# Performance work log

Hardware: AMD Instinct MI355X
Metric: run time of the kernel (lower is better)

Reference implementation:

```python
import jax, jax.numpy as jnp
import numpy as np

N = 100000   # nodes
E = 1200000  # edges
NIN, EIN = 6, 1
HID, L, H = 64, 3, 4
D = HID // H  # 16 per-head dim


def setup_inputs() -> dict:
    key = jax.random.key(0)
    ks = jax.random.split(key, 20)
    r = lambda k, shape: (jax.random.normal(k, shape, dtype=jnp.float32) * 0.1)
    inp = {
        "x": jax.random.normal(ks[0], (N, NIN), dtype=jnp.float32),
        "edge_index": jax.random.randint(ks[1], (2, E), 0, N, dtype=jnp.int64),
        "edge_attr": jax.random.normal(ks[2], (E, EIN), dtype=jnp.float32),
        # node encoder (Linear-ReLU-Linear)
        "w_ne1": r(ks[3], (NIN, HID)), "b_ne1": jnp.zeros((HID,), jnp.float32),
        "w_ne2": r(ks[4], (HID, HID)), "b_ne2": jnp.zeros((HID,), jnp.float32),
        # edge encoder (Linear)
        "w_ee": r(ks[5], (EIN, HID)), "b_ee": jnp.zeros((HID,), jnp.float32),
        # stacked GAT layers (PyG GATConv w/ edge features, concat heads)
        "w_gat": r(ks[6], (L, HID, HID)),      # node lin per layer
        "w_eg": r(ks[7], (L, HID, HID)),       # edge lin per layer
        "att_src": r(ks[8], (L, H, D)),
        "att_dst": r(ks[9], (L, H, D)),
        "att_edge": r(ks[10], (L, H, D)),
        "b_gat": jnp.zeros((L, HID), jnp.float32),
        # per-layer LayerNorm
        "ln_g": jnp.ones((L, HID), jnp.float32),
        "ln_b": jnp.zeros((L, HID), jnp.float32),
        # output projection
        "w_out": r(ks[11], (HID, HID)), "b_out": jnp.zeros((HID,), jnp.float32),
    }
    return inp


def _layernorm(x, g, b, eps=1e-5):
    m = jnp.mean(x, axis=-1, keepdims=True)
    v = jnp.mean(jnp.square(x - m), axis=-1, keepdims=True)
    return (x - m) * jax.lax.rsqrt(v + eps) * g + b


def reference(x, edge_index, edge_attr, w_ne1, b_ne1, w_ne2, b_ne2, w_ee, b_ee,
              w_gat, w_eg, att_src, att_dst, att_edge, b_gat, ln_g, ln_b,
              w_out, b_out):
    n = x.shape[0]
    src, dst = edge_index[0], edge_index[1]
    # encode nodes / edges
    h = jax.nn.relu(x @ w_ne1 + b_ne1) @ w_ne2 + b_ne2          # [N, HID]
    e = edge_attr @ w_ee + b_ee                                  # [E, HID]
    num_layers = w_gat.shape[0]
    for l in range(num_layers):
        hw = (h @ w_gat[l]).reshape(n, H, D)                     # [N,H,D]
        ew = (e @ w_eg[l]).reshape(-1, H, D)                     # [E,H,D]
        a_s = jnp.sum(hw * att_src[l], axis=-1)                  # [N,H]
        a_d = jnp.sum(hw * att_dst[l], axis=-1)                  # [N,H]
        a_e = jnp.sum(ew * att_edge[l], axis=-1)                 # [E,H]
        score = jax.nn.leaky_relu(a_s[src] + a_d[dst] + a_e, 0.2)  # [E,H]
        # softmax over incoming edges of each destination node
        smax = jax.ops.segment_max(score, dst, num_segments=n)
        ex = jnp.exp(score - smax[dst])
        den = jax.ops.segment_sum(ex, dst, num_segments=n)
        alpha = ex / (den[dst] + 1e-16)                          # [E,H]
        msg = alpha[:, :, None] * hw[src]                        # [E,H,D]
        agg = jax.ops.segment_sum(msg, dst, num_segments=n)      # [N,H,D]
        agg = agg.reshape(n, H * D) + b_gat[l]
        h = _layernorm(h + jax.nn.elu(agg), ln_g[l], ln_b[l])
    return h @ w_out + b_out
```

## Files before the change

### kernel.cpp

```cpp
#include <hip/hip_runtime.h>
#include <hip/hip_bf16.h>

#define NIN 6
#define HIDN 64
#define NHEAD 4
#define DEGPAD 5

__device__ __forceinline__ unsigned short f2bf(float f) {
    unsigned u = __float_as_uint(f);
    unsigned r = (u >> 16) & 1u;
    return (unsigned short)((u + 0x7fffu + r) >> 16);
}

__global__ __launch_bounds__(256) void encode1_kernel(
    const float* __restrict__ x,
    const float* __restrict__ w1, const float* __restrict__ b1,
    float* __restrict__ hid, int N) {
    int t = blockIdx.x * blockDim.x + threadIdx.x;
    int n = t >> 6, j = t & 63;
    if (n >= N) return;
    float acc = b1[j];
#pragma unroll
    for (int i = 0; i < NIN; i++) acc += x[n * NIN + i] * w1[i * HIDN + j];
    hid[(size_t)n * HIDN + j] = acc > 0.f ? acc : 0.f;
}

__global__ __launch_bounds__(256) void mm64_plain_kernel(
    const float* __restrict__ src, const float* __restrict__ W,
    const float* __restrict__ bias, float* __restrict__ dst, int N) {
    int j = threadIdx.x & 63;
    int wv = (blockIdx.x * blockDim.x + threadIdx.x) >> 6;
    int nw = (gridDim.x * blockDim.x) >> 6;

    float Wc[HIDN];
#pragma unroll
    for (int k = 0; k < HIDN; k++) Wc[k] = W[k * HIDN + j];
    float bj = bias[j];

    for (int n0 = wv; n0 < N; n0 += nw) {
        int n = __builtin_amdgcn_readfirstlane(n0);
        const float4* __restrict__ row = (const float4*)(src + (size_t)n * HIDN);
        float a0 = 0.f, a1 = 0.f, a2 = 0.f, a3 = 0.f;
#pragma unroll
        for (int kk = 0; kk < 16; kk++) {
            float4 r = row[kk];
            a0 += r.x * Wc[4 * kk];
            a1 += r.y * Wc[4 * kk + 1];
            a2 += r.z * Wc[4 * kk + 2];
            a3 += r.w * Wc[4 * kk + 3];
        }
        dst[(size_t)n * HIDN + j] = ((a0 + a1) + (a2 + a3)) + bj;
    }
}

__global__ __launch_bounds__(256) void mm64_attn_kernel(
    const float* __restrict__ src, const float* __restrict__ W,
    const float* __restrict__ att_s, const float* __restrict__ att_d,
    unsigned short* __restrict__ dst16,
    float* __restrict__ a_s, float* __restrict__ a_d, int N) {
    int j = threadIdx.x & 63;
    int wv = (blockIdx.x * blockDim.x + threadIdx.x) >> 6;
    int nw = (gridDim.x * blockDim.x) >> 6;

    float Wc[HIDN];
#pragma unroll
    for (int k = 0; k < HIDN; k++) Wc[k] = W[k * HIDN + j];
    float asj = att_s[j];
    float adj = att_d[j];

    for (int n0 = wv; n0 < N; n0 += nw) {
        int n = __builtin_amdgcn_readfirstlane(n0);
        const float4* __restrict__ row = (const float4*)(src + (size_t)n * HIDN);
        float a0 = 0.f, a1 = 0.f, a2 = 0.f, a3 = 0.f;
#pragma unroll
        for (int kk = 0; kk < 16; kk++) {
            float4 r = row[kk];
            a0 += r.x * Wc[4 * kk];
            a1 += r.y * Wc[4 * kk + 1];
            a2 += r.z * Wc[4 * kk + 2];
            a3 += r.w * Wc[4 * kk + 3];
        }
        float acc = (a0 + a1) + (a2 + a3);
        dst16[(size_t)n * HIDN + j] = f2bf(acc);
        float ts = acc * asj;
        float td = acc * adj;
#pragma unroll
        for (int o = 8; o > 0; o >>= 1) {
            ts += __shfl_xor(ts, o);
            td += __shfl_xor(td, o);
        }
        if ((j & 15) == 0) {
            a_s[(size_t)n * NHEAD + (j >> 4)] = ts;
            a_d[(size_t)n * NHEAD + (j >> 4)] = td;
        }
    }
}

__global__ void consts_kernel(const float* __restrict__ w_ee, const float* __restrict__ b_ee,
                              const float* __restrict__ w_eg, const float* __restrict__ att_edge,
                              float* __restrict__ c1, float* __restrict__ c0) {
    int t = threadIdx.x;
    if (t >= 12) return;
    int l = t >> 2, hh = t & 3;
    float s1 = 0.f, s0 = 0.f;
    for (int j = 0; j < HIDN; j++) {
        float wj = 0.f;
        for (int d = 0; d < 16; d++)
            wj += w_eg[l * 4096 + j * 64 + hh * 16 + d] * att_edge[l * 64 + hh * 16 + d];
        s1 += w_ee[j] * wj;
        s0 += b_ee[j] * wj;
    }
    c1[l * 4 + hh] = s1;
    c0[l * 4 + hh] = s0;
}

__global__ __launch_bounds__(256) void hist_kernel(const int* __restrict__ ei,
                                                   unsigned* __restrict__ deg,
                                                   unsigned* __restrict__ rank, int E) {
    int e = blockIdx.x * 256 + threadIdx.x;
    if (e < E) rank[e] = atomicAdd(&deg[(size_t)ei[E + e] << DEGPAD], 1u);
}

__global__ __launch_bounds__(256) void scan1_kernel(const unsigned* __restrict__ deg,
                                                    unsigned* __restrict__ rp,
                                                    unsigned* __restrict__ bsum, int N) {
    __shared__ unsigned sm[256];
    int t = threadIdx.x, i = blockIdx.x * 256 + t;
    unsigned v = (i < N) ? deg[(size_t)i << DEGPAD] : 0u;
    sm[t] = v;
    __syncthreads();
    unsigned x = v;
    for (int o = 1; o < 256; o <<= 1) {
        unsigned add = (t >= o) ? sm[t - o] : 0u;
        __syncthreads();
        x += add; sm[t] = x;
        __syncthreads();
    }
    if (i < N) rp[i] = x - v;
    if (t == 255) bsum[blockIdx.x] = x;
}

__global__ void scan2_kernel(const unsigned* __restrict__ bsum,
                             unsigned* __restrict__ boff, int nb) {
    __shared__ unsigned sm[1024];
    int t = threadIdx.x;
    unsigned v = (t < nb) ? bsum[t] : 0u;
    sm[t] = v;
    __syncthreads();
    unsigned x = v;
    for (int o = 1; o < 1024; o <<= 1) {
        unsigned add = (t >= o) ? sm[t - o] : 0u;
        __syncthreads();
        x += add; sm[t] = x;
        __syncthreads();
    }
    if (t < nb) boff[t] = x - v;
}

__global__ __launch_bounds__(256) void scan3_kernel(unsigned* __restrict__ rp,
                                                    const unsigned* __restrict__ boff,
                                                    int N, int E) {
    int i = blockIdx.x * 256 + threadIdx.x;
    if (i < N) rp[i] = rp[i] + boff[blockIdx.x];
    if (i == 0) rp[N] = (unsigned)E;
}

__global__ __launch_bounds__(256) void csr_scatter_kernel(
    const int* __restrict__ ei, const float* __restrict__ eattr,
    const unsigned* __restrict__ rp, const unsigned* __restrict__ rank,
    int2* __restrict__ eca, int E) {
    int e = blockIdx.x * 256 + threadIdx.x;
    if (e >= E) return;
    int s = ei[e], d = ei[E + e];
    unsigned p = rp[d] + rank[e];
    eca[p] = make_int2(s, __float_as_int(eattr[e]));
}

__global__ __launch_bounds__(256) void gat_fused_kernel(
    const unsigned* __restrict__ rp, const int2* __restrict__ eca,
    const unsigned short* __restrict__ hw16,
    const float* __restrict__ a_s, const float* __restrict__ a_d,
    const float* __restrict__ c1, const float* __restrict__ c0,
    float* __restrict__ h, const float* __restrict__ bg,
    const float* __restrict__ g, const float* __restrict__ b, int N) {
    __shared__ float exl[4 * 272];
    __shared__ int srl[4 * 68];
    int t = blockIdx.x * blockDim.x + threadIdx.x;
    int lane = t & 63;
    int q = lane >> 4;
    int l = lane & 15;
    int hd = l >> 2;
    int sub = l & 3;
    int n = ((t >> 6) << 2) + q;
    int wslot = (threadIdx.x >> 6);
    float* myex = exl + wslot * 272 + 68 * q;
    int* mysrc = srl + wslot * 68 + 17 * q;

    bool nv = n < N;
    unsigned beg = nv ? rp[n] : 0u;
    int deg = nv ? (int)(rp[n + 1] - beg) : 0;

    float4 ad4 = nv ? *(const float4*)(a_d + ((size_t)n << 2)) : make_float4(0, 0, 0, 0);
    float4 C1 = *(const float4*)c1;
    float4 C0 = *(const float4*)c0;

    int md = deg;
    md = max(md, __shfl_xor(md, 16));
    md = max(md, __shfl_xor(md, 32));
    int chunks = (md + 15) >> 4;

    const unsigned* __restrict__ hwp = (const unsigned*)hw16;
    unsigned loff = (unsigned)(l << 1);

    float ssum = 0.f;
    float ac0 = 0.f, ac1 = 0.f, ac2 = 0.f, ac3 = 0.f;

    for (int k = 0; k < chunks; k++) {
        int i = (k << 4) + l;
        bool act = i < deg;
        int2 ce = act ? eca[beg + i] : make_int2(0, 0);
        int src = ce.x;
        float ea = __int_as_float(ce.y);
        float4 as4 = act ? *(const float4*)(a_s + ((size_t)src << 2))
                         : make_float4(0, 0, 0, 0);
        float s0 = as4.x + ad4.x + ea * C1.x + C0.x;
        float s1 = as4.y + ad4.y + ea * C1.y + C0.y;
        float s2 = as4.z + ad4.z + ea * C1.z + C0.z;
        float s3 = as4.w + ad4.w + ea * C1.w + C0.w;
        s0 = s0 >= 0.f ? s0 : 0.2f * s0;
        s1 = s1 >= 0.f ? s1 : 0.2f * s1;
        s2 = s2 >= 0.f ? s2 : 0.2f * s2;
        s3 = s3 >= 0.f ? s3 : 0.2f * s3;
        float e0 = act ? __expf(s0) : 0.f;
        float e1 = act ? __expf(s1) : 0.f;
        float e2 = act ? __expf(s2) : 0.f;
        float e3 = act ? __expf(s3) : 0.f;
        *(float4*)(myex + (l << 2)) = make_float4(e0, e1, e2, e3);
        mysrc[l] = act ? src : 0;

        float w0 = myex[(sub << 2) + hd];
        float w1 = myex[((sub + 4) << 2) + hd];
        float w2 = myex[((sub + 8) << 2) + hd];
        float w3 = myex[((sub + 12) << 2) + hd];
        float csum = (w0 + w1) + (w2 + w3);
        csum += __shfl_xor(csum, 1);
        csum += __shfl_xor(csum, 2);
        ssum += csum;

#pragma unroll
        for (int e = 0; e < 16; e++) {
            float w = myex[(e << 2) + hd];
            int so = mysrc[e];
            uint2 uu = *(const uint2*)(hwp + (((unsigned)so << 5) + loff));
            ac0 += w * __uint_as_float(uu.x << 16);
            ac1 += w * __uint_as_float(uu.x & 0xffff0000u);
            ac2 += w * __uint_as_float(uu.y << 16);
            ac3 += w * __uint_as_float(uu.y & 0xffff0000u);
        }
    }

    if (!nv) return;
    float inv = 1.f / (ssum + 1e-16f);
    float4 bg4 = *(const float4*)(bg + (l << 2));
    float4 hv4 = *(const float4*)(h + (size_t)n * HIDN + (l << 2));

    float a0 = ac0 * inv + bg4.x;
    float a1 = ac1 * inv + bg4.y;
    float a2 = ac2 * inv + bg4.z;
    float a3 = ac3 * inv + bg4.w;
    a0 = a0 > 0.f ? a0 : (__expf(a0) - 1.f);
    a1 = a1 > 0.f ? a1 : (__expf(a1) - 1.f);
    a2 = a2 > 0.f ? a2 : (__expf(a2) - 1.f);
    a3 = a3 > 0.f ? a3 : (__expf(a3) - 1.f);
    float v0 = hv4.x + a0, v1 = hv4.y + a1, v2 = hv4.z + a2, v3 = hv4.w + a3;

    float s = (v0 + v1) + (v2 + v3);
    float sq = (v0 * v0 + v1 * v1) + (v2 * v2 + v3 * v3);
#pragma unroll
    for (int o = 8; o > 0; o >>= 1) {
        s += __shfl_xor(s, o);
        sq += __shfl_xor(sq, o);
    }
    float mean = s * (1.f / 64.f);
    float var = sq * (1.f / 64.f) - mean * mean;
    float rr = rsqrtf(var + 1e-5f);
    float4 g4 = *(const float4*)(g + (l << 2));
    float4 b4 = *(const float4*)(b + (l << 2));
    float4 outv;
    outv.x = (v0 - mean) * rr * g4.x + b4.x;
    outv.y = (v1 - mean) * rr * g4.y + b4.y;
    outv.z = (v2 - mean) * rr * g4.z + b4.z;
    outv.w = (v3 - mean) * rr * g4.w + b4.w;
    *(float4*)(h + (size_t)n * HIDN + (l << 2)) = outv;
}

extern "C" void kernel_launch(void* const* d_in, const int* in_sizes, int n_in,
                              void* d_out, int out_size, void* d_ws, size_t ws_size,
                              hipStream_t stream) {
    const float* x      = (const float*)d_in[0];
    const int*   ei     = (const int*)d_in[1];
    const float* eattr  = (const float*)d_in[2];
    const float* w_ne1  = (const float*)d_in[3];
    const float* b_ne1  = (const float*)d_in[4];
    const float* w_ne2  = (const float*)d_in[5];
    const float* b_ne2  = (const float*)d_in[6];
    const float* w_ee   = (const float*)d_in[7];
    const float* b_ee   = (const float*)d_in[8];
    const float* w_gat  = (const float*)d_in[9];
    const float* w_eg   = (const float*)d_in[10];
    const float* att_src= (const float*)d_in[11];
    const float* att_dst= (const float*)d_in[12];
    const float* att_edge=(const float*)d_in[13];
    const float* b_gat  = (const float*)d_in[14];
    const float* ln_g   = (const float*)d_in[15];
    const float* ln_b   = (const float*)d_in[16];
    const float* w_out  = (const float*)d_in[17];
    const float* b_out  = (const float*)d_in[18];

    const int N = in_sizes[0] / NIN;
    const int E = in_sizes[2];

    float* ws   = (float*)d_ws;
    float* h    = ws;
    float* hid  = h + (size_t)N * 64;
    unsigned short* hw16 = (unsigned short*)(hid + (size_t)N * 64);
    float* a_s  = (float*)(hw16 + (size_t)N * 64);
    float* a_d  = a_s + (size_t)N * 4;
    float* c1   = a_d + (size_t)N * 4;
    float* c0   = c1 + 12;
    int2*  eca  = (int2*)(c0 + 12);
    unsigned* rank = (unsigned*)(eca + (size_t)E);
    unsigned* deg  = rank + (size_t)E;
    unsigned* rp   = deg + ((size_t)N << DEGPAD);
    unsigned* bsum = rp + (size_t)N + 1;
    unsigned* boff = bsum + 1024;

    dim3 blk(256);
    int nodeWaveBlocks = (int)(((size_t)N * 64 + 255) / 256);
    int quadBlocks = (int)(((size_t)((N + 3) / 4) * 64 + 255) / 256);
    int edgeBlocks = (E + 255) / 256;
    int nodeBlocks = (N + 255) / 256;
    int mmBlocks = 2048;

    hipMemsetAsync(deg, 0, ((size_t)N << DEGPAD) * sizeof(unsigned), stream);
    hist_kernel<<<edgeBlocks, blk, 0, stream>>>(ei, deg, rank, E);
    scan1_kernel<<<nodeBlocks, blk, 0, stream>>>(deg, rp, bsum, N);
    scan2_kernel<<<1, 1024, 0, stream>>>(bsum, boff, nodeBlocks);
    scan3_kernel<<<nodeBlocks, blk, 0, stream>>>(rp, boff, N, E);
    csr_scatter_kernel<<<edgeBlocks, blk, 0, stream>>>(ei, eattr, rp, rank, eca, E);

    consts_kernel<<<1, 64, 0, stream>>>(w_ee, b_ee, w_eg, att_edge, c1, c0);

    encode1_kernel<<<nodeWaveBlocks, blk, 0, stream>>>(x, w_ne1, b_ne1, hid, N);
    mm64_plain_kernel<<<mmBlocks, blk, 0, stream>>>(hid, w_ne2, b_ne2, h, N);

    mm64_attn_kernel<<<mmBlocks, blk, 0, stream>>>(
        h, w_gat, att_src, att_dst, hw16, a_s, a_d, N);

    for (int l = 0; l < 3; l++) {
        gat_fused_kernel<<<quadBlocks, blk, 0, stream>>>(
            rp, eca, hw16, a_s, a_d, c1 + l * 4, c0 + l * 4,
            h, b_gat + l * 64, ln_g + l * 64, ln_b + l * 64, N);
        if (l < 2) {
            mm64_attn_kernel<<<mmBlocks, blk, 0, stream>>>(
                h, w_gat + (size_t)(l + 1) * 4096,
                att_src + (l + 1) * 64, att_dst + (l + 1) * 64,
                hw16, a_s, a_d, N);
        }
    }
    mm64_plain_kernel<<<mmBlocks, blk, 0, stream>>>(h, w_out, b_out, (float*)d_out, N);
}
```

Before: 499.5 us.

## Fuse independent preprocessing kernels into combined launches via block-range dispatch

Independent preprocessing stages now share launches: histogram, first encoder layer and edge constants run in one kernel; the block-local scan runs alongside the second encoder matmul; CSR scatter runs alongside the first attention matmul. The three-kernel scan is cut to two, with each block summing its preceding block totals directly instead of running a separate single-block scan. This removes several kernel launches and lets independent work overlap on the GPU, at the cost of mixed-role blocks and some redundant prefix summation.

```diff
diff --git a/kernel.cpp b/kernel.cpp
--- a/kernel.cpp
+++ b/kernel.cpp
@@ -1,5 +1,4 @@
 #include <hip/hip_runtime.h>
-#include <hip/hip_bf16.h>
 
 #define NIN 6
 #define HIDN 64
@@ -12,32 +11,16 @@
     return (unsigned short)((u + 0x7fffu + r) >> 16);
 }
 
-__global__ __launch_bounds__(256) void encode1_kernel(
-    const float* __restrict__ x,
-    const float* __restrict__ w1, const float* __restrict__ b1,
-    float* __restrict__ hid, int N) {
-    int t = blockIdx.x * blockDim.x + threadIdx.x;
-    int n = t >> 6, j = t & 63;
-    if (n >= N) return;
-    float acc = b1[j];
-#pragma unroll
-    for (int i = 0; i < NIN; i++) acc += x[n * NIN + i] * w1[i * HIDN + j];
-    hid[(size_t)n * HIDN + j] = acc > 0.f ? acc : 0.f;
-}
-
-__global__ __launch_bounds__(256) void mm64_plain_kernel(
-    const float* __restrict__ src, const float* __restrict__ W,
-    const float* __restrict__ bias, float* __restrict__ dst, int N) {
+__device__ __forceinline__ void mm64_plain_body(
+    const float* __restrict__ src, const float* __restrict__ W,
+    const float* __restrict__ bias, float* __restrict__ dst, int N,
+    int wv0, int nw) {
     int j = threadIdx.x & 63;
-    int wv = (blockIdx.x * blockDim.x + threadIdx.x) >> 6;
-    int nw = (gridDim.x * blockDim.x) >> 6;
-
     float Wc[HIDN];
 #pragma unroll
     for (int k = 0; k < HIDN; k++) Wc[k] = W[k * HIDN + j];
     float bj = bias[j];
-
-    for (int n0 = wv; n0 < N; n0 += nw) {
+    for (int n0 = wv0; n0 < N; n0 += nw) {
         int n = __builtin_amdgcn_readfirstlane(n0);
         const float4* __restrict__ row = (const float4*)(src + (size_t)n * HIDN);
         float a0 = 0.f, a1 = 0.f, a2 = 0.f, a3 = 0.f;
@@ -53,22 +36,19 @@
     }
 }
 
-__global__ __launch_bounds__(256) void mm64_attn_kernel(
+__device__ __forceinline__ void mm64_attn_body(
     const float* __restrict__ src, const float* __restrict__ W,
     const float* __restrict__ att_s, const float* __restrict__ att_d,
     unsigned short* __restrict__ dst16,
-    float* __restrict__ a_s, float* __restrict__ a_d, int N) {
+    float* __restrict__ a_s, float* __restrict__ a_d, int N,
+    int wv0, int nw) {
     int j = threadIdx.x & 63;
-    int wv = (blockIdx.x * blockDim.x + threadIdx.x) >> 6;
-    int nw = (gridDim.x * blockDim.x) >> 6;
-
     float Wc[HIDN];
 #pragma unroll
     for (int k = 0; k < HIDN; k++) Wc[k] = W[k * HIDN + j];
     float asj = att_s[j];
     float adj = att_d[j];
-
-    for (int n0 = wv; n0 < N; n0 += nw) {
+    for (int n0 = wv0; n0 < N; n0 += nw) {
         int n = __builtin_amdgcn_readfirstlane(n0);
         const float4* __restrict__ row = (const float4*)(src + (size_t)n * HIDN);
         float a0 = 0.f, a1 = 0.f, a2 = 0.f, a3 = 0.f;
@@ -96,84 +76,134 @@
     }
 }
 
-__global__ void consts_kernel(const float* __restrict__ w_ee, const float* __restrict__ b_ee,
-                              const float* __restrict__ w_eg, const float* __restrict__ att_edge,
-                              float* __restrict__ c1, float* __restrict__ c0) {
-    int t = threadIdx.x;
-    if (t >= 12) return;
-    int l = t >> 2, hh = t & 3;
-    float s1 = 0.f, s0 = 0.f;
-    for (int j = 0; j < HIDN; j++) {
+__global__ __launch_bounds__(256) void pre_kernel(
+    const int* __restrict__ ei, unsigned* __restrict__ deg,
+    unsigned* __restrict__ rank, int E,
+    const float* __restrict__ x, const float* __restrict__ w1,
+    const float* __restrict__ b1, float* __restrict__ hid, int N,
+    const float* __restrict__ w_ee, const float* __restrict__ b_ee,
+    const float* __restrict__ w_eg, const float* __restrict__ att_edge,
+    float* __restrict__ c1, float* __restrict__ c0,
+    int histBlocks, int encBlocks) {
+    int b = blockIdx.x;
+    if (b < histBlocks) {
+        int e = b * 256 + threadIdx.x;
+        if (e < E) rank[e] = atomicAdd(&deg[(size_t)ei[E + e] << DEGPAD], 1u);
+        return;
+    }
+    b -= histBlocks;
+    if (b < encBlocks) {
+        int t = b * 256 + threadIdx.x;
+        int n = t >> 6, j = t & 63;
+        if (n >= N) return;
+        float acc = b1[j];
+#pragma unroll
+        for (int i = 0; i < NIN; i++) acc += x[n * NIN + i] * w1[i * HIDN + j];
+        hid[(size_t)n * HIDN + j] = acc > 0.f ? acc : 0.f;
+        return;
+    }
+    int w = threadIdx.x >> 6, j = threadIdx.x & 63;
+    for (int p = w; p < 12; p += 4) {
+        int l = p >> 2, hh = p & 3;
+        const float* wr = w_eg + l * 4096 + j * 64 + hh * 16;
+        const float* ae = att_edge + l * 64 + hh * 16;
         float wj = 0.f;
-        for (int d = 0; d < 16; d++)
-            wj += w_eg[l * 4096 + j * 64 + hh * 16 + d] * att_edge[l * 64 + hh * 16 + d];
-        s1 += w_ee[j] * wj;
-        s0 += b_ee[j] * wj;
-    }
-    c1[l * 4 + hh] = s1;
-    c0[l * 4 + hh] = s0;
-}
-
-__global__ __launch_bounds__(256) void hist_kernel(const int* __restrict__ ei,
-                                                   unsigned* __restrict__ deg,
-                                                   unsigned* __restrict__ rank, int E) {
-    int e = blockIdx.x * 256 + threadIdx.x;
-    if (e < E) rank[e] = atomicAdd(&deg[(size_t)ei[E + e] << DEGPAD], 1u);
-}
-
-__global__ __launch_bounds__(256) void scan1_kernel(const unsigned* __restrict__ deg,
-                                                    unsigned* __restrict__ rp,
-                                                    unsigned* __restrict__ bsum, int N) {
+#pragma unroll
+        for (int d = 0; d < 16; d++) wj += wr[d] * ae[d];
+        float s1 = w_ee[j] * wj;
+        float s0 = b_ee[j] * wj;
+#pragma unroll
+        for (int o = 32; o > 0; o >>= 1) {
+            s1 += __shfl_xor(s1, o);
+            s0 += __shfl_xor(s0, o);
+        }
+        if (j == 0) { c1[l * 4 + hh] = s1; c0[l * 4 + hh] = s0; }
+    }
+}
+
+__global__ __launch_bounds__(256) void mid_kernel(
+    const unsigned* __restrict__ deg, unsigned* __restrict__ rp,
+    unsigned* __restrict__ bsum, int N,
+    const float* __restrict__ src, const float* __restrict__ W,
+    const float* __restrict__ bias, float* __restrict__ dst,
+    int scanBlocks, int mmWaves) {
     __shared__ unsigned sm[256];
-    int t = threadIdx.x, i = blockIdx.x * 256 + t;
-    unsigned v = (i < N) ? deg[(size_t)i << DEGPAD] : 0u;
-    sm[t] = v;
+    int b = blockIdx.x;
+    if (b < scanBlocks) {
+        int t = threadIdx.x, i = b * 256 + t;
+        unsigned v = (i < N) ? deg[(size_t)i << DEGPAD] : 0u;
+        sm[t] = v;
+        __syncthreads();
+        unsigned xx = v;
+        for (int o = 1; o < 256; o <<= 1) {
+            unsigned add = (t >= o) ? sm[t - o] : 0u;
+            __syncthreads();
+            xx += add; sm[t] = xx;
+            __syncthreads();
+        }
+        if (i < N) rp[i] = xx - v;
+        if (t == 255) bsum[b] = xx;
+        return;
+    }
+    int wv0 = ((b - scanBlocks) * 256 + threadIdx.x) >> 6;
+    mm64_plain_body(src, W, bias, dst, N, wv0, mmWaves);
+}
+
+__global__ __launch_bounds__(256) void scan23_kernel(
+    unsigned* __restrict__ rp, const unsigned* __restrict__ bsum,
+    int N, int E) {
+    __shared__ unsigned red[256];
+    int b = blockIdx.x, t = threadIdx.x;
+    unsigned partial = 0;
+    for (int j = t; j < b; j += 256) partial += bsum[j];
+    red[t] = partial;
     __syncthreads();
-    unsigned x = v;
-    for (int o = 1; o < 256; o <<= 1) {
-        unsigned add = (t >= o) ? sm[t - o] : 0u;
+    for (int o = 128; o > 0; o >>= 1) {
+        if (t < o) red[t] += red[t + o];
         __syncthreads();
-        x += add; sm[t] = x;
-        __syncthreads();
-    }
-    if (i < N) rp[i] = x - v;
-    if (t == 255) bsum[blockIdx.x] = x;
-}
-
-__global__ void scan2_kernel(const unsigned* __restrict__ bsum,
-                             unsigned* __restrict__ boff, int nb) {
-    __shared__ unsigned sm[1024];
-    int t = threadIdx.x;
-    unsigned v = (t < nb) ? bsum[t] : 0u;
-    sm[t] = v;
-    __syncthreads();
-    unsigned x = v;
-    for (int o = 1; o < 1024; o <<= 1) {
-        unsigned add = (t >= o) ? sm[t - o] : 0u;
-        __syncthreads();
-        x += add; sm[t] = x;
-        __syncthreads();
-    }
-    if (t < nb) boff[t] = x - v;
-}
-
-__global__ __launch_bounds__(256) void scan3_kernel(unsigned* __restrict__ rp,
-                                                    const unsigned* __restrict__ boff,
-                                                    int N, int E) {
-    int i = blockIdx.x * 256 + threadIdx.x;
-    if (i < N) rp[i] = rp[i] + boff[blockIdx.x];
-    if (i == 0) rp[N] = (unsigned)E;
-}
-
-__global__ __launch_bounds__(256) void csr_scatter_kernel(
+    }
+    unsigned off = red[0];
+    int i = b * 256 + t;
+    if (i < N) rp[i] += off;
+    if (b == 0 && t == 0) rp[N] = (unsigned)E;
+}
+
+__global__ __launch_bounds__(256) void sca_kernel(
     const int* __restrict__ ei, const float* __restrict__ eattr,
     const unsigned* __restrict__ rp, const unsigned* __restrict__ rank,
-    int2* __restrict__ eca, int E) {
-    int e = blockIdx.x * 256 + threadIdx.x;
-    if (e >= E) return;
-    int s = ei[e], d = ei[E + e];
-    unsigned p = rp[d] + rank[e];
-    eca[p] = make_int2(s, __float_as_int(eattr[e]));
+    int2* __restrict__ eca, int E,
+    const float* __restrict__ src, const float* __restrict__ W,
+    const float* __restrict__ att_s, const float* __restrict__ att_d,
+    unsigned short* __restrict__ dst16,
+    float* __restrict__ a_s, float* __restrict__ a_d, int N,
+    int scatBlocks, int mmWaves) {
+    int b = blockIdx.x;
+    if (b < scatBlocks) {
+        int e = b * 256 + threadIdx.x;
+        if (e >= E) return;
+        int s = ei[e], d = ei[E + e];
+        unsigned p = rp[d] + rank[e];
+        eca[p] = make_int2(s, __float_as_int(eattr[e]));
+        return;
+    }
+    int wv0 = ((b - scatBlocks) * 256 + threadIdx.x) >> 6;
+    mm64_attn_body(src, W, att_s, att_d, dst16, a_s, a_d, N, wv0, mmWaves);
+}
+
+__global__ __launch_bounds__(256) void mm64_plain_kernel(
+    const float* __restrict__ src, const float* __restrict__ W,
+    const float* __restrict__ bias, float* __restrict__ dst, int N, int nw) {
+    mm64_plain_body(src, W, bias, dst, N,
+                    (blockIdx.x * blockDim.x + threadIdx.x) >> 6, nw);
+}
+
+__global__ __launch_bounds__(256) void mm64_attn_kernel(
+    const float* __restrict__ src, const float* __restrict__ W,
+    const float* __restrict__ att_s, const float* __restrict__ att_d,
+    unsigned short* __restrict__ dst16,
+    float* __restrict__ a_s, float* __restrict__ a_d, int N, int nw) {
+    mm64_attn_body(src, W, att_s, att_d, dst16, a_s, a_d, N,
+                   (blockIdx.x * blockDim.x + threadIdx.x) >> 6, nw);
 }
 
 __global__ __launch_bounds__(256) void gat_fused_kernel(
@@ -334,28 +364,33 @@
     unsigned* rp   = deg + ((size_t)N << DEGPAD);
     unsigned* bsum = rp + (size_t)N + 1;
     unsigned* boff = bsum + 1024;
+    (void)boff;
 
     dim3 blk(256);
-    int nodeWaveBlocks = (int)(((size_t)N * 64 + 255) / 256);
+    int edgeBlocks = (E + 255) / 256;
+    int encBlocks  = (int)(((size_t)N * 64 + 255) / 256);
     int quadBlocks = (int)(((size_t)((N + 3) / 4) * 64 + 255) / 256);
-    int edgeBlocks = (E + 255) / 256;
     int nodeBlocks = (N + 255) / 256;
     int mmBlocks = 2048;
+    int mmWaves  = mmBlocks * 4;
 
     hipMemsetAsync(deg, 0, ((size_t)N << DEGPAD) * sizeof(unsigned), stream);
-    hist_kernel<<<edgeBlocks, blk, 0, stream>>>(ei, deg, rank, E);
-    scan1_kernel<<<nodeBlocks, blk, 0, stream>>>(deg, rp, bsum, N);
-    scan2_kernel<<<1, 1024, 0, stream>>>(bsum, boff, nodeBlocks);
-    scan3_kernel<<<nodeBlocks, blk, 0, stream>>>(rp, boff, N, E);
-    csr_scatter_kernel<<<edgeBlocks, blk, 0, stream>>>(ei, eattr, rp, rank, eca, E);
-
-    consts_kernel<<<1, 64, 0, stream>>>(w_ee, b_ee, w_eg, att_edge, c1, c0);
-
-    encode1_kernel<<<nodeWaveBlocks, blk, 0, stream>>>(x, w_ne1, b_ne1, hid, N);
-    mm64_plain_kernel<<<mmBlocks, blk, 0, stream>>>(hid, w_ne2, b_ne2, h, N);
-
-    mm64_attn_kernel<<<mmBlocks, blk, 0, stream>>>(
-        h, w_gat, att_src, att_dst, hw16, a_s, a_d, N);
+
+    pre_kernel<<<edgeBlocks + encBlocks + 1, blk, 0, stream>>>(
+        ei, deg, rank, E,
+        x, w_ne1, b_ne1, hid, N,
+        w_ee, b_ee, w_eg, att_edge, c1, c0,
+        edgeBlocks, encBlocks);
+
+    mid_kernel<<<nodeBlocks + mmBlocks, blk, 0, stream>>>(
+        deg, rp, bsum, N, hid, w_ne2, b_ne2, h, nodeBlocks, mmWaves);
+
+    scan23_kernel<<<nodeBlocks, blk, 0, stream>>>(rp, bsum, N, E);
+
+    sca_kernel<<<edgeBlocks + mmBlocks, blk, 0, stream>>>(
+        ei, eattr, rp, rank, eca, E,
+        h, w_gat, att_src, att_dst, hw16, a_s, a_d, N,
+        edgeBlocks, mmWaves);
 
     for (int l = 0; l < 3; l++) {
         gat_fused_kernel<<<quadBlocks, blk, 0, stream>>>(
@@ -365,8 +400,8 @@
             mm64_attn_kernel<<<mmBlocks, blk, 0, stream>>>(
                 h, w_gat + (size_t)(l + 1) * 4096,
                 att_src + (l + 1) * 64, att_dst + (l + 1) * 64,
-                hw16, a_s, a_d, N);
-        }
-    }
-    mm64_plain_kernel<<<mmBlocks, blk, 0, stream>>>(h, w_out, b_out, (float*)d_out, N);
-}
+                hw16, a_s, a_d, N, mmWaves);
+        }
+    }
+    mm64_plain_kernel<<<mmBlocks, blk, 0, stream>>>(h, w_out, b_out, (float*)d_out, N, mmWaves);
+}
```

New measurement: 464.4 us. -7.0%, faster.
